# Kernel optimization log

Measured on AMD Instinct MI355X. Metric: run time of the kernel, lower is better.

The kernel has to match this reference:

```python
import jax, jax.numpy as jnp
import numpy as np

N = 30000          # nodes
R = 8              # relations
NUM_BASES = 30     # basis decomposition (fixed in module)
IN_DIM = 256
Z_DIM = 128
HID = Z_DIM * 2
E = N * 16         # edges (avg degree 16)


def setup_inputs() -> dict:
    key = jax.random.key(0)
    ks = jax.random.split(key, 12)
    x = jax.random.normal(ks[0], (N, IN_DIM), jnp.float32)
    edge_index = jax.random.randint(ks[1], (2, E), 0, N, dtype=jnp.int64)
    edge_type = jax.random.randint(ks[2], (E,), 0, R, dtype=jnp.int64)
    s1 = 1.0 / np.sqrt(IN_DIM)
    s2 = 1.0 / np.sqrt(HID)
    sb = 1.0 / np.sqrt(NUM_BASES)
    bases1 = jax.random.normal(ks[3], (NUM_BASES, IN_DIM, HID), jnp.float32) * s1
    comp1 = jax.random.normal(ks[4], (R, NUM_BASES), jnp.float32) * sb
    root1 = jax.random.normal(ks[5], (IN_DIM, HID), jnp.float32) * s1
    bias1 = jnp.zeros((HID,), jnp.float32)
    bases2 = jax.random.normal(ks[6], (NUM_BASES, HID, Z_DIM), jnp.float32) * s2
    comp2 = jax.random.normal(ks[7], (R, NUM_BASES), jnp.float32) * sb
    root2 = jax.random.normal(ks[8], (HID, Z_DIM), jnp.float32) * s2
    bias2 = jnp.zeros((Z_DIM,), jnp.float32)
    return dict(x=x, edge_index=edge_index, edge_type=edge_type,
                bases1=bases1, comp1=comp1, root1=root1, bias1=bias1,
                bases2=bases2, comp2=comp2, root2=root2, bias2=bias2)


def _rgcn_layer(x, src, dst, etype, bases, comp, root, bias):
    # weight[r] = sum_b comp[r,b] * bases[b]  (basis decomposition)
    n = x.shape[0]
    W = jnp.einsum('rb,bio->rio', comp, bases)          # [R, in, out]
    xall = jnp.einsum('ni,rio->nro', x, W)              # [N, R, out] dense transform
    msg = xall[src, etype]                              # [E, out] gather per edge
    seg = dst * R + etype                               # segment = (dst, relation)
    sums = jax.ops.segment_sum(msg, seg, num_segments=n * R)
    cnt = jax.ops.segment_sum(jnp.ones((msg.shape[0],), msg.dtype), seg,
                              num_segments=n * R)
    mean = sums / jnp.maximum(cnt, 1.0)[:, None]        # PyG RGCNConv aggr='mean'
    agg = mean.reshape(n, R, -1).sum(axis=1)            # sum over relations
    return agg + x @ root + bias


def reference(x, edge_index, edge_type, bases1, comp1, root1, bias1,
              bases2, comp2, root2, bias2):
    src, dst = edge_index[0], edge_index[1]
    z = _rgcn_layer(x, src, dst, edge_type, bases1, comp1, root1, bias1)
    z = jax.nn.leaky_relu(z, negative_slope=0.01)
    z = _rgcn_layer(z, src, dst, edge_type, bases2, comp2, root2, bias2)
    return z
```

## Files before the change

### kernel.cpp

```cpp
#include <hip/hip_runtime.h>
#include <hip/hip_bf16.h>
#include <stdint.h>

#define NN     30000
#define MPAD   30080
#define RR     8
#define NBASES 30
#define KD     256
#define EE     480000
#define NSEG   (NN * RR)
#define K1     2048
#define KTOT   2304
#define BK     64
#define CAP    32

typedef unsigned short u16;
typedef __attribute__((ext_vector_type(8))) short bf16x8;
typedef __attribute__((ext_vector_type(4))) float f32x4;

__device__ __forceinline__ u16 f2b(float f) {
  union { float f; uint32_t u; } v; v.f = f;
  return (u16)((v.u + 0x7fffu + ((v.u >> 16) & 1u)) >> 16);
}
__device__ __forceinline__ float b2f(u16 h) {
  union { uint32_t u; float f; } v; v.u = ((uint32_t)h) << 16;
  return v.f;
}

__device__ __forceinline__ void gl_lds16(const void* g, void* l) {
  __builtin_amdgcn_global_load_lds((__attribute__((address_space(1))) void*)g,
                                   (__attribute__((address_space(3))) void*)l,
                                   16, 0, 0);
}

template<int NT, bool LAST>
__global__ __launch_bounds__(512, 6)
void k_gemm8w(const u16* __restrict__ A1, const u16* __restrict__ A2,
              const u16* __restrict__ BT, const float* __restrict__ bias,
              u16* __restrict__ ob, float* __restrict__ of) {
  constexpr int NI = NT / 32;
  constexpr int NKI = KTOT / BK;
  __shared__ u16 Alds[2][64 * BK];
  __shared__ u16 Blds[2][NT * BK];
  const int tid = threadIdx.x;
  const int w = tid >> 6, lane = tid & 63;
  const int bn = blockIdx.x * NT, bm = blockIdx.y * 64;
  const int wm = (w >> 1) * 16;
  const int wn = (w & 1) * (NT / 2);
  const int l15 = lane & 15, l4 = lane >> 4;

  f32x4 acc[NI];
  #pragma unroll
  for (int ni = 0; ni < NI; ++ni) acc[ni] = (f32x4){0.f, 0.f, 0.f, 0.f};

  auto stage = [&](int buf, int k0) {
    {
      int chb = w * 64;
      int ch = chb + lane;
      int row = ch >> 3, pc = ch & 7;
      int lc = pc ^ (row & 7);
      const u16* src = (k0 < K1)
          ? &A1[(size_t)(bm + row) * K1 + k0 + lc * 8]
          : &A2[(size_t)(bm + row) * KD + (k0 - K1) + lc * 8];
      gl_lds16(src, &Alds[buf][chb * 8]);
    }
    #pragma unroll
    for (int it = 0; it < NT / 64; ++it) {
      int chb = it * 512 + w * 64;
      int ch = chb + lane;
      int row = ch >> 3, pc = ch & 7;
      int lc = pc ^ (row & 7);
      gl_lds16(&BT[(size_t)(bn + row) * KTOT + k0 + lc * 8], &Blds[buf][chb * 8]);
    }
  };

  stage(0, 0);
  __syncthreads();
  int cur = 0;
  for (int t = 0; t < NKI; ++t) {
    if (t + 1 < NKI) stage(cur ^ 1, (t + 1) * BK);
    #pragma unroll
    for (int s = 0; s < 2; ++s) {
      bf16x8 av, bv[NI];
      {
        int row = wm + l15;
        int pc = (4 * s + l4) ^ (row & 7);
        av = *(const bf16x8*)&Alds[cur][row * BK + pc * 8];
      }
      #pragma unroll
      for (int ni = 0; ni < NI; ++ni) {
        int row = wn + ni * 16 + l15;
        int pc = (4 * s + l4) ^ (row & 7);
        bv[ni] = *(const bf16x8*)&Blds[cur][row * BK + pc * 8];
      }
      #pragma unroll
      for (int ni = 0; ni < NI; ++ni)
        acc[ni] = __builtin_amdgcn_mfma_f32_16x16x32_bf16(av, bv[ni], acc[ni], 0, 0, 0);
    }
    __syncthreads();
    cur ^= 1;
  }

  #pragma unroll
  for (int ni = 0; ni < NI; ++ni) {
    int col = bn + wn + ni * 16 + l15;
    float bb = bias[col];
    #pragma unroll
    for (int v = 0; v < 4; ++v) {
      int row = bm + wm + l4 * 4 + v;
      float val = acc[ni][v] + bb;
      if (!LAST) {
        val = val > 0.f ? val : 0.01f * val;
        ob[(size_t)row * KD + col] = f2b(val);
      } else if (row < NN) {
        of[(size_t)row * 128 + col] = val;
      }
    }
  }
}

__global__ __launch_bounds__(256)
void k_mean(const u16* __restrict__ X, const int* __restrict__ cnt,
            const int* __restrict__ esrc, u16* __restrict__ H) {
  const int d = blockIdx.x;
  const int tid = threadIdx.x;
  const int r = tid >> 5;
  const int ln = tid & 31;
  const int s = (d << 3) + r;
  int n = cnt[s]; n = n < CAP ? n : CAP;
  const int base = s * CAP;

  float a0 = 0.f, a1 = 0.f, a2 = 0.f, a3 = 0.f;
  float a4 = 0.f, a5 = 0.f, a6 = 0.f, a7 = 0.f;
  #pragma unroll 1
  for (int e = 0; e < n; e += 2) {
    int s0 = esrc[base + e];
    bool has1 = (e + 1 < n);
    int s1 = has1 ? esrc[base + e + 1] : s0;
    uint4 v0 = *(const uint4*)&X[(size_t)s0 * KD + ln * 8];
    uint4 v1 = *(const uint4*)&X[(size_t)s1 * KD + ln * 8];
    a0 += b2f((u16)v0.x); a1 += b2f((u16)(v0.x >> 16));
    a2 += b2f((u16)v0.y); a3 += b2f((u16)(v0.y >> 16));
    a4 += b2f((u16)v0.z); a5 += b2f((u16)(v0.z >> 16));
    a6 += b2f((u16)v0.w); a7 += b2f((u16)(v0.w >> 16));
    float m = has1 ? 1.f : 0.f;
    a0 = fmaf(m, b2f((u16)v1.x), a0); a1 = fmaf(m, b2f((u16)(v1.x >> 16)), a1);
    a2 = fmaf(m, b2f((u16)v1.y), a2); a3 = fmaf(m, b2f((u16)(v1.y >> 16)), a3);
    a4 = fmaf(m, b2f((u16)v1.z), a4); a5 = fmaf(m, b2f((u16)(v1.z >> 16)), a5);
    a6 = fmaf(m, b2f((u16)v1.w), a6); a7 = fmaf(m, b2f((u16)(v1.w >> 16)), a7);
  }
  float sc = (n > 0) ? 1.f / (float)n : 0.f;
  uint4 o;
  o.x = ((uint32_t)f2b(a1 * sc) << 16) | (uint32_t)f2b(a0 * sc);
  o.y = ((uint32_t)f2b(a3 * sc) << 16) | (uint32_t)f2b(a2 * sc);
  o.z = ((uint32_t)f2b(a5 * sc) << 16) | (uint32_t)f2b(a4 * sc);
  o.w = ((uint32_t)f2b(a7 * sc) << 16) | (uint32_t)f2b(a6 * sc);
  *(uint4*)&H[(size_t)d * K1 + (r << 8) + ln * 8] = o;
}

__global__ void k_cast_x(const float* __restrict__ x, u16* __restrict__ xb) {
  int t = blockIdx.x * 256 + threadIdx.x;
  if (t < NN * KD / 4) {
    float4 v = ((const float4*)x)[t];
    union { u16 h[4]; uint2 u; } p;
    p.h[0] = f2b(v.x); p.h[1] = f2b(v.y); p.h[2] = f2b(v.z); p.h[3] = f2b(v.w);
    ((uint2*)xb)[t] = p.u;
  }
}

__global__ void k_combine1(const float* __restrict__ bases, const float* __restrict__ comp,
                           const float* __restrict__ root, u16* __restrict__ BT) {
  int k = blockIdx.x, o = threadIdx.x;
  float v;
  if (k < K1) {
    int r = k >> 8, i = k & 255;
    float acc = 0.f;
    #pragma unroll
    for (int b = 0; b < NBASES; ++b)
      acc += comp[r * NBASES + b] * bases[(size_t)b * 65536 + i * 256 + o];
    v = acc;
  } else {
    v = root[(k - K1) * 256 + o];
  }
  BT[(size_t)o * KTOT + k] = f2b(v);
}

__global__ void k_combine2(const float* __restrict__ bases, const float* __restrict__ comp,
                           const float* __restrict__ root, u16* __restrict__ BT) {
  int k = blockIdx.x, o = threadIdx.x;
  float v;
  if (k < K1) {
    int r = k >> 8, i = k & 255;
    float acc = 0.f;
    #pragma unroll
    for (int b = 0; b < NBASES; ++b)
      acc += comp[r * NBASES + b] * bases[(size_t)b * 32768 + i * 128 + o];
    v = acc;
  } else {
    v = root[(k - K1) * 128 + o];
  }
  BT[(size_t)o * KTOT + k] = f2b(v);
}

__global__ void k_bucket_fs(const int* __restrict__ ei, const int* __restrict__ ety,
                            int* __restrict__ cnt, int* __restrict__ esrc) {
  int e = blockIdx.x * 256 + threadIdx.x;
  if (e < EE) {
    int seg = ei[EE + e] * RR + ety[e];
    int pos = atomicAdd(&cnt[seg], 1);
    if (pos < CAP) esrc[seg * CAP + pos] = ei[e];
  }
}

extern "C" void kernel_launch(void* const* d_in, const int* in_sizes, int n_in,
                              void* d_out, int out_size, void* d_ws, size_t ws_size,
                              hipStream_t stream) {
  const float* x      = (const float*)d_in[0];
  const int*   ei     = (const int*)d_in[1];
  const int*   ety    = (const int*)d_in[2];
  const float* bases1 = (const float*)d_in[3];
  const float* comp1  = (const float*)d_in[4];
  const float* root1  = (const float*)d_in[5];
  const float* bias1  = (const float*)d_in[6];
  const float* bases2 = (const float*)d_in[7];
  const float* comp2  = (const float*)d_in[8];
  const float* root2  = (const float*)d_in[9];
  const float* bias2  = (const float*)d_in[10];
  float* out = (float*)d_out;

  char* p = (char*)d_ws;
  auto alloc = [&](size_t bytes) {
    char* q = p; p += (bytes + 255) & ~(size_t)255; return q;
  };
  u16* H    = (u16*)alloc((size_t)MPAD * K1 * 2);
  u16* xb   = (u16*)alloc((size_t)MPAD * KD * 2);
  u16* z1b  = (u16*)alloc((size_t)MPAD * KD * 2);
  u16* BT1  = (u16*)alloc((size_t)256 * KTOT * 2);
  u16* BT2  = (u16*)alloc((size_t)128 * KTOT * 2);
  int* cnt  = (int*)alloc((size_t)NSEG * 4);
  int* esrc = (int*)alloc((size_t)NSEG * CAP * 4);

  hipMemsetAsync(cnt, 0, (size_t)NSEG * 4, stream);
  k_bucket_fs<<<(EE + 255) / 256, 256, 0, stream>>>(ei, ety, cnt, esrc);

  k_cast_x<<<NN * KD / 4 / 256, 256, 0, stream>>>(x, xb);
  k_combine1<<<KTOT, 256, 0, stream>>>(bases1, comp1, root1, BT1);
  k_combine2<<<KTOT, 128, 0, stream>>>(bases2, comp2, root2, BT2);

  k_mean<<<NN, 256, 0, stream>>>(xb, cnt, esrc, H);
  k_gemm8w<128, false><<<dim3(2, 470), 512, 0, stream>>>(H, xb, BT1, bias1, z1b, nullptr);

  k_mean<<<NN, 256, 0, stream>>>(z1b, cnt, esrc, H);
  k_gemm8w<64, true><<<dim3(2, 470), 512, 0, stream>>>(H, z1b, BT2, bias2, nullptr, out);
}
```

Measured before the change: 376.1 us.

## Fuse neighbor mean aggregation into GEMM A-tile construction

Removes the separate mean-aggregation kernel and its 30000x2048 bf16 intermediate buffer. Each GEMM block now gathers and averages neighbor rows on the fly to build the A tile in LDS, overlapped with the MFMA work on the previous tile. The second layer uses a single 128-wide N tile so the gather is not duplicated across column blocks. The first layer still runs two column blocks, so the gather work is done twice there, and the gather sits on the GEMM's critical path with lower occupancy.

After: 461.9 us. +22.8%, slower.

```diff
diff --git a/kernel.cpp b/kernel.cpp
--- a/kernel.cpp
+++ b/kernel.cpp
@@ -34,36 +34,39 @@
 }
 
 template<int NT, bool LAST>
-__global__ __launch_bounds__(512, 6)
-void k_gemm8w(const u16* __restrict__ A1, const u16* __restrict__ A2,
-              const u16* __restrict__ BT, const float* __restrict__ bias,
-              u16* __restrict__ ob, float* __restrict__ of) {
+__global__ __launch_bounds__(512, 4)
+void k_fused(const u16* __restrict__ X, const int* __restrict__ cnt,
+             const int* __restrict__ esrc, const u16* __restrict__ BT,
+             const float* __restrict__ bias, u16* __restrict__ ob,
+             float* __restrict__ of) {
   constexpr int NI = NT / 32;
   constexpr int NKI = KTOT / BK;
   __shared__ u16 Alds[2][64 * BK];
   __shared__ u16 Blds[2][NT * BK];
+  __shared__ int   cntL[512];
+  __shared__ float invL[512];
   const int tid = threadIdx.x;
   const int w = tid >> 6, lane = tid & 63;
   const int bn = blockIdx.x * NT, bm = blockIdx.y * 64;
   const int wm = (w >> 1) * 16;
   const int wn = (w & 1) * (NT / 2);
   const int l15 = lane & 15, l4 = lane >> 4;
+  const int grow = tid >> 3, goc = tid & 7;
 
   f32x4 acc[NI];
   #pragma unroll
   for (int ni = 0; ni < NI; ++ni) acc[ni] = (f32x4){0.f, 0.f, 0.f, 0.f};
 
-  auto stage = [&](int buf, int k0) {
-    {
-      int chb = w * 64;
-      int ch = chb + lane;
-      int row = ch >> 3, pc = ch & 7;
-      int lc = pc ^ (row & 7);
-      const u16* src = (k0 < K1)
-          ? &A1[(size_t)(bm + row) * K1 + k0 + lc * 8]
-          : &A2[(size_t)(bm + row) * KD + (k0 - K1) + lc * 8];
-      gl_lds16(src, &Alds[buf][chb * 8]);
-    }
+  {
+    int gd = bm + grow;
+    int n = 0;
+    if (gd < NN) n = cnt[(gd << 3) + (tid & 7)];
+    n = n < CAP ? n : CAP;
+    cntL[tid] = n;
+    invL[tid] = (n > 0) ? 1.f / (float)n : 0.f;
+  }
+
+  auto stage_B = [&](int buf, int k0) {
     #pragma unroll
     for (int it = 0; it < NT / 64; ++it) {
       int chb = it * 512 + w * 64;
@@ -74,31 +77,87 @@
     }
   };
 
-  stage(0, 0);
+  auto stage_Aroot = [&](int buf, int k0) {
+    int chb = w * 64;
+    int ch = chb + lane;
+    int row = ch >> 3, pc = ch & 7;
+    int lc = pc ^ (row & 7);
+    gl_lds16(&X[(size_t)(bm + row) * KD + (k0 - K1) + lc * 8], &Alds[buf][chb * 8]);
+  };
+
+  auto abuild = [&](int k0, uint4& o) {
+    int r = k0 >> 8;
+    int c0 = (k0 & 255) + goc * 8;
+    int sL = (grow << 3) + r;
+    int n = cntL[sL];
+    float inv = invL[sL];
+    int base = (((bm + grow) << 3) + r) * CAP;
+    float a0 = 0.f, a1 = 0.f, a2 = 0.f, a3 = 0.f;
+    float a4 = 0.f, a5 = 0.f, a6 = 0.f, a7 = 0.f;
+    #pragma unroll 1
+    for (int e = 0; e < n; e += 2) {
+      int s0 = esrc[base + e];
+      bool has1 = (e + 1 < n);
+      int s1 = has1 ? esrc[base + e + 1] : s0;
+      uint4 v0 = *(const uint4*)&X[(size_t)s0 * KD + c0];
+      uint4 v1 = *(const uint4*)&X[(size_t)s1 * KD + c0];
+      a0 += b2f((u16)v0.x); a1 += b2f((u16)(v0.x >> 16));
+      a2 += b2f((u16)v0.y); a3 += b2f((u16)(v0.y >> 16));
+      a4 += b2f((u16)v0.z); a5 += b2f((u16)(v0.z >> 16));
+      a6 += b2f((u16)v0.w); a7 += b2f((u16)(v0.w >> 16));
+      float m = has1 ? 1.f : 0.f;
+      a0 = fmaf(m, b2f((u16)v1.x), a0); a1 = fmaf(m, b2f((u16)(v1.x >> 16)), a1);
+      a2 = fmaf(m, b2f((u16)v1.y), a2); a3 = fmaf(m, b2f((u16)(v1.y >> 16)), a3);
+      a4 = fmaf(m, b2f((u16)v1.z), a4); a5 = fmaf(m, b2f((u16)(v1.z >> 16)), a5);
+      a6 = fmaf(m, b2f((u16)v1.w), a6); a7 = fmaf(m, b2f((u16)(v1.w >> 16)), a7);
+    }
+    o.x = ((uint32_t)f2b(a1 * inv) << 16) | (uint32_t)f2b(a0 * inv);
+    o.y = ((uint32_t)f2b(a3 * inv) << 16) | (uint32_t)f2b(a2 * inv);
+    o.z = ((uint32_t)f2b(a5 * inv) << 16) | (uint32_t)f2b(a4 * inv);
+    o.w = ((uint32_t)f2b(a7 * inv) << 16) | (uint32_t)f2b(a6 * inv);
+  };
+  auto awrite = [&](int buf, uint4 o) {
+    *(uint4*)&Alds[buf][grow * BK + (goc ^ (grow & 7)) * 8] = o;
+  };
+
+  stage_B(0, 0);
   __syncthreads();
-  int cur = 0;
+  {
+    uint4 o0; abuild(0, o0); awrite(0, o0);
+  }
+  __syncthreads();
+
+  int buf = 0;
   for (int t = 0; t < NKI; ++t) {
-    if (t + 1 < NKI) stage(cur ^ 1, (t + 1) * BK);
+    const bool pf = (t + 1 < NKI);
+    const int kn = (t + 1) * BK;
+    uint4 o; bool og = false;
+    if (pf) {
+      stage_B(buf ^ 1, kn);
+      if (kn < K1) { abuild(kn, o); og = true; }
+      else stage_Aroot(buf ^ 1, kn);
+    }
     #pragma unroll
     for (int s = 0; s < 2; ++s) {
       bf16x8 av, bv[NI];
       {
         int row = wm + l15;
         int pc = (4 * s + l4) ^ (row & 7);
-        av = *(const bf16x8*)&Alds[cur][row * BK + pc * 8];
+        av = *(const bf16x8*)&Alds[buf][row * BK + pc * 8];
       }
       #pragma unroll
       for (int ni = 0; ni < NI; ++ni) {
         int row = wn + ni * 16 + l15;
         int pc = (4 * s + l4) ^ (row & 7);
-        bv[ni] = *(const bf16x8*)&Blds[cur][row * BK + pc * 8];
+        bv[ni] = *(const bf16x8*)&Blds[buf][row * BK + pc * 8];
       }
       #pragma unroll
       for (int ni = 0; ni < NI; ++ni)
         acc[ni] = __builtin_amdgcn_mfma_f32_16x16x32_bf16(av, bv[ni], acc[ni], 0, 0, 0);
     }
+    if (og) awrite(buf ^ 1, o);
     __syncthreads();
-    cur ^= 1;
+    buf ^= 1;
   }
 
   #pragma unroll
@@ -117,45 +176,6 @@
       }
     }
   }
-}
-
-__global__ __launch_bounds__(256)
-void k_mean(const u16* __restrict__ X, const int* __restrict__ cnt,
-            const int* __restrict__ esrc, u16* __restrict__ H) {
-  const int d = blockIdx.x;
-  const int tid = threadIdx.x;
-  const int r = tid >> 5;
-  const int ln = tid & 31;
-  const int s = (d << 3) + r;
-  int n = cnt[s]; n = n < CAP ? n : CAP;
-  const int base = s * CAP;
-
-  float a0 = 0.f, a1 = 0.f, a2 = 0.f, a3 = 0.f;
-  float a4 = 0.f, a5 = 0.f, a6 = 0.f, a7 = 0.f;
-  #pragma unroll 1
-  for (int e = 0; e < n; e += 2) {
-    int s0 = esrc[base + e];
-    bool has1 = (e + 1 < n);
-    int s1 = has1 ? esrc[base + e + 1] : s0;
-    uint4 v0 = *(const uint4*)&X[(size_t)s0 * KD + ln * 8];
-    uint4 v1 = *(const uint4*)&X[(size_t)s1 * KD + ln * 8];
-    a0 += b2f((u16)v0.x); a1 += b2f((u16)(v0.x >> 16));
-    a2 += b2f((u16)v0.y); a3 += b2f((u16)(v0.y >> 16));
-    a4 += b2f((u16)v0.z); a5 += b2f((u16)(v0.z >> 16));
-    a6 += b2f((u16)v0.w); a7 += b2f((u16)(v0.w >> 16));
-    float m = has1 ? 1.f : 0.f;
-    a0 = fmaf(m, b2f((u16)v1.x), a0); a1 = fmaf(m, b2f((u16)(v1.x >> 16)), a1);
-    a2 = fmaf(m, b2f((u16)v1.y), a2); a3 = fmaf(m, b2f((u16)(v1.y >> 16)), a3);
-    a4 = fmaf(m, b2f((u16)v1.z), a4); a5 = fmaf(m, b2f((u16)(v1.z >> 16)), a5);
-    a6 = fmaf(m, b2f((u16)v1.w), a6); a7 = fmaf(m, b2f((u16)(v1.w >> 16)), a7);
-  }
-  float sc = (n > 0) ? 1.f / (float)n : 0.f;
-  uint4 o;
-  o.x = ((uint32_t)f2b(a1 * sc) << 16) | (uint32_t)f2b(a0 * sc);
-  o.y = ((uint32_t)f2b(a3 * sc) << 16) | (uint32_t)f2b(a2 * sc);
-  o.z = ((uint32_t)f2b(a5 * sc) << 16) | (uint32_t)f2b(a4 * sc);
-  o.w = ((uint32_t)f2b(a7 * sc) << 16) | (uint32_t)f2b(a6 * sc);
-  *(uint4*)&H[(size_t)d * K1 + (r << 8) + ln * 8] = o;
 }
 
 __global__ void k_cast_x(const float* __restrict__ x, u16* __restrict__ xb) {
@@ -232,7 +252,6 @@
   auto alloc = [&](size_t bytes) {
     char* q = p; p += (bytes + 255) & ~(size_t)255; return q;
   };
-  u16* H    = (u16*)alloc((size_t)MPAD * K1 * 2);
   u16* xb   = (u16*)alloc((size_t)MPAD * KD * 2);
   u16* z1b  = (u16*)alloc((size_t)MPAD * KD * 2);
   u16* BT1  = (u16*)alloc((size_t)256 * KTOT * 2);
@@ -247,9 +266,7 @@
   k_combine1<<<KTOT, 256, 0, stream>>>(bases1, comp1, root1, BT1);
   k_combine2<<<KTOT, 128, 0, stream>>>(bases2, comp2, root2, BT2);
 
-  k_mean<<<NN, 256, 0, stream>>>(xb, cnt, esrc, H);
-  k_gemm8w<128, false><<<dim3(2, 470), 512, 0, stream>>>(H, xb, BT1, bias1, z1b, nullptr);
-
-  k_mean<<<NN, 256, 0, stream>>>(z1b, cnt, esrc, H);
-  k_gemm8w<64, true><<<dim3(2, 470), 512, 0, stream>>>(H, z1b, BT2, bias2, nullptr, out);
-}
+  k_fused<128, false><<<dim3(2, 470), 512, 0, stream>>>(xb, cnt, esrc, BT1, bias1, z1b, nullptr);
+
+  k_fused<128, true><<<dim3(1, 470), 512, 0, stream>>>(z1b, cnt, esrc, BT2, bias2, nullptr, out);
+}
```

## Reorder RGCN layers to transform first, then aggregate per-relation outputs

Applied to the files above, without the earlier changes.

The order of work in each layer is flipped. Before, neighbour features were mean-aggregated per relation into a wide K=2304 buffer and then multiplied by the stacked weights. Now each node is first transformed by all relation weights plus the root weight into a wide Y buffer, using short-K GEMMs with an LDS-staged, coalesced bf16 epilogue. A gather kernel then averages Y rows per (dst, relation), sums over relations and adds the root term, bias and activation. This halves the per-edge gather width in layer 2 and drops the long-K GEMM, at the cost of writing a large intermediate Y and running GEMMs with only four K-steps each.

After: 374.4 us. About the same (-0.5%).

```diff
diff --git a/kernel.cpp b/kernel.cpp
--- a/kernel.cpp
+++ b/kernel.cpp
@@ -9,10 +9,10 @@
 #define KD     256
 #define EE     480000
 #define NSEG   (NN * RR)
-#define K1     2048
-#define KTOT   2304
 #define BK     64
 #define CAP    32
+#define NC1    2304
+#define NC2    1152
 
 typedef unsigned short u16;
 typedef __attribute__((ext_vector_type(8))) short bf16x8;
@@ -33,20 +33,22 @@
                                    16, 0, 0);
 }
 
-template<int NT, bool LAST>
+template<int NCOLS>
 __global__ __launch_bounds__(512, 6)
-void k_gemm8w(const u16* __restrict__ A1, const u16* __restrict__ A2,
-              const u16* __restrict__ BT, const float* __restrict__ bias,
-              u16* __restrict__ ob, float* __restrict__ of) {
-  constexpr int NI = NT / 32;
-  constexpr int NKI = KTOT / BK;
-  __shared__ u16 Alds[2][64 * BK];
-  __shared__ u16 Blds[2][NT * BK];
+void k_gemm_y(const u16* __restrict__ A, const u16* __restrict__ Bn,
+              u16* __restrict__ Y) {
+  constexpr int NT = 128;
+  constexpr int NI = 4;
+  constexpr int NKI = KD / BK;
+  __shared__ __align__(16) char smem[49152];
+  u16 (*Alds)[64 * BK] = (u16(*)[64 * BK])smem;
+  u16 (*Blds)[NT * BK] = (u16(*)[NT * BK])(smem + 2 * 64 * BK * 2);
+  float* eps = (float*)smem;
   const int tid = threadIdx.x;
   const int w = tid >> 6, lane = tid & 63;
   const int bn = blockIdx.x * NT, bm = blockIdx.y * 64;
   const int wm = (w >> 1) * 16;
-  const int wn = (w & 1) * (NT / 2);
+  const int wn = (w & 1) * 64;
   const int l15 = lane & 15, l4 = lane >> 4;
 
   f32x4 acc[NI];
@@ -59,103 +61,124 @@
       int ch = chb + lane;
       int row = ch >> 3, pc = ch & 7;
       int lc = pc ^ (row & 7);
-      const u16* src = (k0 < K1)
-          ? &A1[(size_t)(bm + row) * K1 + k0 + lc * 8]
-          : &A2[(size_t)(bm + row) * KD + (k0 - K1) + lc * 8];
-      gl_lds16(src, &Alds[buf][chb * 8]);
-    }
-    #pragma unroll
-    for (int it = 0; it < NT / 64; ++it) {
+      gl_lds16(&A[(size_t)(bm + row) * KD + k0 + lc * 8], &Alds[buf][chb * 8]);
+    }
+    #pragma unroll
+    for (int it = 0; it < 2; ++it) {
       int chb = it * 512 + w * 64;
       int ch = chb + lane;
       int row = ch >> 3, pc = ch & 7;
       int lc = pc ^ (row & 7);
-      gl_lds16(&BT[(size_t)(bn + row) * KTOT + k0 + lc * 8], &Blds[buf][chb * 8]);
+      gl_lds16(&Bn[(size_t)(bn + row) * KD + k0 + lc * 8], &Blds[buf][chb * 8]);
     }
   };
 
   stage(0, 0);
   __syncthreads();
-  int cur = 0;
+  int buf = 0;
   for (int t = 0; t < NKI; ++t) {
-    if (t + 1 < NKI) stage(cur ^ 1, (t + 1) * BK);
+    if (t + 1 < NKI) stage(buf ^ 1, (t + 1) * BK);
     #pragma unroll
     for (int s = 0; s < 2; ++s) {
       bf16x8 av, bv[NI];
       {
         int row = wm + l15;
         int pc = (4 * s + l4) ^ (row & 7);
-        av = *(const bf16x8*)&Alds[cur][row * BK + pc * 8];
+        av = *(const bf16x8*)&Alds[buf][row * BK + pc * 8];
       }
       #pragma unroll
       for (int ni = 0; ni < NI; ++ni) {
         int row = wn + ni * 16 + l15;
         int pc = (4 * s + l4) ^ (row & 7);
-        bv[ni] = *(const bf16x8*)&Blds[cur][row * BK + pc * 8];
+        bv[ni] = *(const bf16x8*)&Blds[buf][row * BK + pc * 8];
       }
       #pragma unroll
       for (int ni = 0; ni < NI; ++ni)
         acc[ni] = __builtin_amdgcn_mfma_f32_16x16x32_bf16(av, bv[ni], acc[ni], 0, 0, 0);
     }
     __syncthreads();
-    cur ^= 1;
+    buf ^= 1;
   }
 
   #pragma unroll
   for (int ni = 0; ni < NI; ++ni) {
-    int col = bn + wn + ni * 16 + l15;
-    float bb = bias[col];
+    int col = wn + ni * 16 + l15;
     #pragma unroll
     for (int v = 0; v < 4; ++v) {
-      int row = bm + wm + l4 * 4 + v;
-      float val = acc[ni][v] + bb;
-      if (!LAST) {
-        val = val > 0.f ? val : 0.01f * val;
-        ob[(size_t)row * KD + col] = f2b(val);
-      } else if (row < NN) {
-        of[(size_t)row * 128 + col] = val;
-      }
-    }
-  }
-}
-
+      int row = wm + l4 * 4 + v;
+      eps[row * 132 + col] = acc[ni][v];
+    }
+  }
+  __syncthreads();
+  {
+    int row = tid >> 3, oc = tid & 7;
+    const float* src = &eps[row * 132 + oc * 16];
+    uint4 o[2];
+    #pragma unroll
+    for (int h = 0; h < 2; ++h) {
+      float f0 = src[h*8+0], f1 = src[h*8+1], f2 = src[h*8+2], f3 = src[h*8+3];
+      float f4 = src[h*8+4], f5 = src[h*8+5], f6 = src[h*8+6], f7 = src[h*8+7];
+      o[h].x = ((uint32_t)f2b(f1) << 16) | (uint32_t)f2b(f0);
+      o[h].y = ((uint32_t)f2b(f3) << 16) | (uint32_t)f2b(f2);
+      o[h].z = ((uint32_t)f2b(f5) << 16) | (uint32_t)f2b(f4);
+      o[h].w = ((uint32_t)f2b(f7) << 16) | (uint32_t)f2b(f6);
+    }
+    u16* dst = &Y[(size_t)(bm + row) * NCOLS + bn + oc * 16];
+    *(uint4*)dst = o[0];
+    *(uint4*)(dst + 8) = o[1];
+  }
+}
+
+template<int D, bool LAST>
 __global__ __launch_bounds__(256)
-void k_mean(const u16* __restrict__ X, const int* __restrict__ cnt,
-            const int* __restrict__ esrc, u16* __restrict__ H) {
-  const int d = blockIdx.x;
-  const int tid = threadIdx.x;
-  const int r = tid >> 5;
-  const int ln = tid & 31;
+void k_agg(const u16* __restrict__ Y, const int* __restrict__ cnt,
+           const int* __restrict__ esrc, const float* __restrict__ bias,
+           u16* __restrict__ ob, float* __restrict__ of) {
+  constexpr int YW = 9 * D;
+  constexpr int CW = D / 32;
+  __shared__ float part[8 * D];
+  const int d = blockIdx.x, tid = threadIdx.x;
+  const int r = tid >> 5, ln = tid & 31;
   const int s = (d << 3) + r;
   int n = cnt[s]; n = n < CAP ? n : CAP;
   const int base = s * CAP;
 
-  float a0 = 0.f, a1 = 0.f, a2 = 0.f, a3 = 0.f;
-  float a4 = 0.f, a5 = 0.f, a6 = 0.f, a7 = 0.f;
+  float a[CW];
+  #pragma unroll
+  for (int j = 0; j < CW; ++j) a[j] = 0.f;
   #pragma unroll 1
-  for (int e = 0; e < n; e += 2) {
-    int s0 = esrc[base + e];
-    bool has1 = (e + 1 < n);
-    int s1 = has1 ? esrc[base + e + 1] : s0;
-    uint4 v0 = *(const uint4*)&X[(size_t)s0 * KD + ln * 8];
-    uint4 v1 = *(const uint4*)&X[(size_t)s1 * KD + ln * 8];
-    a0 += b2f((u16)v0.x); a1 += b2f((u16)(v0.x >> 16));
-    a2 += b2f((u16)v0.y); a3 += b2f((u16)(v0.y >> 16));
-    a4 += b2f((u16)v0.z); a5 += b2f((u16)(v0.z >> 16));
-    a6 += b2f((u16)v0.w); a7 += b2f((u16)(v0.w >> 16));
-    float m = has1 ? 1.f : 0.f;
-    a0 = fmaf(m, b2f((u16)v1.x), a0); a1 = fmaf(m, b2f((u16)(v1.x >> 16)), a1);
-    a2 = fmaf(m, b2f((u16)v1.y), a2); a3 = fmaf(m, b2f((u16)(v1.y >> 16)), a3);
-    a4 = fmaf(m, b2f((u16)v1.z), a4); a5 = fmaf(m, b2f((u16)(v1.z >> 16)), a5);
-    a6 = fmaf(m, b2f((u16)v1.w), a6); a7 = fmaf(m, b2f((u16)(v1.w >> 16)), a7);
-  }
-  float sc = (n > 0) ? 1.f / (float)n : 0.f;
-  uint4 o;
-  o.x = ((uint32_t)f2b(a1 * sc) << 16) | (uint32_t)f2b(a0 * sc);
-  o.y = ((uint32_t)f2b(a3 * sc) << 16) | (uint32_t)f2b(a2 * sc);
-  o.z = ((uint32_t)f2b(a5 * sc) << 16) | (uint32_t)f2b(a4 * sc);
-  o.w = ((uint32_t)f2b(a7 * sc) << 16) | (uint32_t)f2b(a6 * sc);
-  *(uint4*)&H[(size_t)d * K1 + (r << 8) + ln * 8] = o;
+  for (int e = 0; e < n; ++e) {
+    int sr = esrc[base + e];
+    const u16* row = &Y[(size_t)sr * YW + r * D + ln * CW];
+    if constexpr (CW == 8) {
+      uint4 v = *(const uint4*)row;
+      a[0] += b2f((u16)v.x); a[1] += b2f((u16)(v.x >> 16));
+      a[2] += b2f((u16)v.y); a[3] += b2f((u16)(v.y >> 16));
+      a[4] += b2f((u16)v.z); a[5] += b2f((u16)(v.z >> 16));
+      a[6] += b2f((u16)v.w); a[7] += b2f((u16)(v.w >> 16));
+    } else {
+      uint2 v = *(const uint2*)row;
+      a[0] += b2f((u16)v.x); a[1] += b2f((u16)(v.x >> 16));
+      a[2] += b2f((u16)v.y); a[3] += b2f((u16)(v.y >> 16));
+    }
+  }
+  float inv = (n > 0) ? 1.f / (float)n : 0.f;
+  #pragma unroll
+  for (int j = 0; j < CW; ++j) part[r * D + ln * CW + j] = a[j] * inv;
+  __syncthreads();
+  if (tid < D) {
+    float v = 0.f;
+    #pragma unroll
+    for (int rr = 0; rr < 8; ++rr) v += part[rr * D + tid];
+    v += b2f(Y[(size_t)d * YW + 8 * D + tid]);
+    v += bias[tid];
+    if (!LAST) {
+      v = v > 0.f ? v : 0.01f * v;
+      ob[(size_t)d * KD + tid] = f2b(v);
+    } else {
+      of[(size_t)d * D + tid] = v;
+    }
+  }
 }
 
 __global__ void k_cast_x(const float* __restrict__ x, u16* __restrict__ xb) {
@@ -168,38 +191,36 @@
   }
 }
 
-__global__ void k_combine1(const float* __restrict__ bases, const float* __restrict__ comp,
-                           const float* __restrict__ root, u16* __restrict__ BT) {
-  int k = blockIdx.x, o = threadIdx.x;
-  float v;
-  if (k < K1) {
-    int r = k >> 8, i = k & 255;
+__global__ void k_combineT1(const float* __restrict__ bases, const float* __restrict__ comp,
+                            const float* __restrict__ root, u16* __restrict__ Bn) {
+  int i = blockIdx.x, rg = blockIdx.y, o = threadIdx.x;
+  float v; int j;
+  if (rg < RR) {
     float acc = 0.f;
     #pragma unroll
     for (int b = 0; b < NBASES; ++b)
-      acc += comp[r * NBASES + b] * bases[(size_t)b * 65536 + i * 256 + o];
-    v = acc;
+      acc += comp[rg * NBASES + b] * bases[(size_t)b * 65536 + i * 256 + o];
+    v = acc; j = rg * 256 + o;
   } else {
-    v = root[(k - K1) * 256 + o];
-  }
-  BT[(size_t)o * KTOT + k] = f2b(v);
-}
-
-__global__ void k_combine2(const float* __restrict__ bases, const float* __restrict__ comp,
-                           const float* __restrict__ root, u16* __restrict__ BT) {
-  int k = blockIdx.x, o = threadIdx.x;
-  float v;
-  if (k < K1) {
-    int r = k >> 8, i = k & 255;
+    v = root[i * 256 + o]; j = 2048 + o;
+  }
+  Bn[(size_t)j * KD + i] = f2b(v);
+}
+
+__global__ void k_combineT2(const float* __restrict__ bases, const float* __restrict__ comp,
+                            const float* __restrict__ root, u16* __restrict__ Bn) {
+  int i = blockIdx.x, rg = blockIdx.y, o = threadIdx.x;
+  float v; int j;
+  if (rg < RR) {
     float acc = 0.f;
     #pragma unroll
     for (int b = 0; b < NBASES; ++b)
-      acc += comp[r * NBASES + b] * bases[(size_t)b * 32768 + i * 128 + o];
-    v = acc;
+      acc += comp[rg * NBASES + b] * bases[(size_t)b * 32768 + i * 128 + o];
+    v = acc; j = rg * 128 + o;
   } else {
-    v = root[(k - K1) * 128 + o];
-  }
-  BT[(size_t)o * KTOT + k] = f2b(v);
+    v = root[i * 128 + o]; j = 1024 + o;
+  }
+  Bn[(size_t)j * KD + i] = f2b(v);
 }
 
 __global__ void k_bucket_fs(const int* __restrict__ ei, const int* __restrict__ ety,
@@ -232,11 +253,11 @@
   auto alloc = [&](size_t bytes) {
     char* q = p; p += (bytes + 255) & ~(size_t)255; return q;
   };
-  u16* H    = (u16*)alloc((size_t)MPAD * K1 * 2);
+  u16* Y    = (u16*)alloc((size_t)MPAD * NC1 * 2);
   u16* xb   = (u16*)alloc((size_t)MPAD * KD * 2);
   u16* z1b  = (u16*)alloc((size_t)MPAD * KD * 2);
-  u16* BT1  = (u16*)alloc((size_t)256 * KTOT * 2);
-  u16* BT2  = (u16*)alloc((size_t)128 * KTOT * 2);
+  u16* Bn1  = (u16*)alloc((size_t)NC1 * KD * 2);
+  u16* Bn2  = (u16*)alloc((size_t)NC2 * KD * 2);
   int* cnt  = (int*)alloc((size_t)NSEG * 4);
   int* esrc = (int*)alloc((size_t)NSEG * CAP * 4);
 
@@ -244,12 +265,12 @@
   k_bucket_fs<<<(EE + 255) / 256, 256, 0, stream>>>(ei, ety, cnt, esrc);
 
   k_cast_x<<<NN * KD / 4 / 256, 256, 0, stream>>>(x, xb);
-  k_combine1<<<KTOT, 256, 0, stream>>>(bases1, comp1, root1, BT1);
-  k_combine2<<<KTOT, 128, 0, stream>>>(bases2, comp2, root2, BT2);
-
-  k_mean<<<NN, 256, 0, stream>>>(xb, cnt, esrc, H);
-  k_gemm8w<128, false><<<dim3(2, 470), 512, 0, stream>>>(H, xb, BT1, bias1, z1b, nullptr);
-
-  k_mean<<<NN, 256, 0, stream>>>(z1b, cnt, esrc, H);
-  k_gemm8w<64, true><<<dim3(2, 470), 512, 0, stream>>>(H, z1b, BT2, bias2, nullptr, out);
-}
+  k_combineT1<<<dim3(256, 9), 256, 0, stream>>>(bases1, comp1, root1, Bn1);
+  k_combineT2<<<dim3(256, 9), 128, 0, stream>>>(bases2, comp2, root2, Bn2);
+
+  k_gemm_y<NC1><<<dim3(NC1 / 128, 470), 512, 0, stream>>>(xb, Bn1, Y);
+  k_agg<256, false><<<NN, 256, 0, stream>>>(Y, cnt, esrc, bias1, z1b, nullptr);
+
+  k_gemm_y<NC2><<<dim3(NC2 / 128, 470), 512, 0, stream>>>(z1b, Bn2, Y);
+  k_agg<128, true><<<NN, 256, 0, stream>>>(Y, cnt, esrc, bias2, nullptr, out);
+}
```
